# Kernel optimization log

Hardware: AMD Instinct MI355X
Metric: run time of the kernel (lower is better)

Reference implementation:

```python
import jax, jax.numpy as jnp
import numpy as np
import math

D_MODEL = 768
NUM_HEADS = 12
HEAD_DIM = D_MODEL // NUM_HEADS
HIDDEN = 3072
EPS = 1e-05
CLAMP = 1e9


def setup_inputs() -> dict:
    key = jax.random.key(0)
    ks = jax.random.split(key, 8)
    s = 0.02
    return {
        "x": jax.random.normal(ks[0], (1, 4096, D_MODEL), dtype=jnp.float32),
        "gamma1": jnp.ones((D_MODEL,), jnp.float32),
        "beta1": jnp.zeros((D_MODEL,), jnp.float32),
        "Wqkv": jax.random.normal(ks[1], (D_MODEL, 3 * D_MODEL), jnp.float32) * s,
        "bqkv": jnp.zeros((3 * D_MODEL,), jnp.float32),
        "Wo": jax.random.normal(ks[2], (D_MODEL, D_MODEL), jnp.float32) * s,
        "bo": jnp.zeros((D_MODEL,), jnp.float32),
        "gamma2": jnp.ones((D_MODEL,), jnp.float32),
        "beta2": jnp.zeros((D_MODEL,), jnp.float32),
        "W1": jax.random.normal(ks[3], (D_MODEL, HIDDEN), jnp.float32) * s,
        "b1": jnp.zeros((HIDDEN,), jnp.float32),
        "W2": jax.random.normal(ks[4], (HIDDEN, D_MODEL), jnp.float32) * s,
        "b2": jnp.zeros((D_MODEL,), jnp.float32),
    }


def layer_norm(x, gamma, beta):
    mean = jnp.mean(x, axis=-1, keepdims=True)
    var = jnp.mean((x - mean) ** 2, axis=-1, keepdims=True)
    y = (x - mean) / jnp.sqrt(var + EPS)
    return gamma * y + beta


def attention_block(x, Wqkv, bqkv, Wo, bo):
    B, S, D = x.shape
    qkv = x @ Wqkv + bqkv                             # [B,S,3D]
    qkv = qkv.reshape(B, S, NUM_HEADS, 3 * HEAD_DIM).transpose(0, 2, 1, 3)  # [B,H,S,3hd]
    q, k, v = jnp.split(qkv, 3, axis=-1)              # each [B,H,S,hd]
    scaled = jnp.einsum("bhqd,bhkd->bhqk", q, k) / math.sqrt(HEAD_DIM)
    causal = jnp.tril(jnp.ones((S, S), dtype=bool))
    scaled = jnp.where(causal, scaled, -jnp.inf)
    scaled = jnp.clip(scaled, -CLAMP, CLAMP)          # torch clamp turns -inf into -1e9
    attn = jax.nn.softmax(scaled, axis=-1)
    vals = jnp.einsum("bhqk,bhkd->bhqd", attn, v)     # [B,H,S,hd]
    vals = vals.transpose(0, 2, 1, 3).reshape(B, S, D)
    return vals @ Wo + bo


def ffn_block(x, W1, b1, W2, b2):
    h = jax.nn.gelu(x @ W1 + b1, approximate=False)
    return h @ W2 + b2


def reference(x, gamma1, beta1, Wqkv, bqkv, Wo, bo, gamma2, beta2, W1, b1, W2, b2):
    x = x + attention_block(layer_norm(x, gamma1, beta1), Wqkv, bqkv, Wo, bo)
    x = x + ffn_block(layer_norm(x, gamma2, beta2), W1, b1, W2, b2)
    return x
```

## Files before the change

### kernel.cpp

```cpp
#include <hip/hip_runtime.h>
#include <hip/hip_bf16.h>
#include <cmath>

using u16 = unsigned short;
typedef __bf16 bf16x8 __attribute__((ext_vector_type(8)));
typedef __bf16 bf16x2 __attribute__((ext_vector_type(2)));
typedef unsigned short u16x8 __attribute__((ext_vector_type(8)));
typedef unsigned short u16x4 __attribute__((ext_vector_type(4)));
typedef float f32x4 __attribute__((ext_vector_type(4)));

#define SEQ 4096
#define DM 768
#define NH 12
#define HD 64
#define HID 3072

__device__ __forceinline__ u16 f2bf(float f) {
    union { float f; unsigned u; } v; v.f = f;
    unsigned r = v.u + 0x7fffu + ((v.u >> 16) & 1u);
    return (u16)(r >> 16);
}

__device__ __forceinline__ unsigned pack_bf16(float a, float b) {
    union { bf16x2 v; unsigned u; } c;
    c.v[0] = (__bf16)a; c.v[1] = (__bf16)b;
    return c.u;
}

__device__ __forceinline__ float gelu_exact(float v) {
    float z = fabsf(v) * 0.70710678118654752f;
    float t = __builtin_amdgcn_rcpf(__builtin_fmaf(0.3275911f, z, 1.0f));
    float p = t * __builtin_fmaf(t, __builtin_fmaf(t, __builtin_fmaf(t,
                __builtin_fmaf(t, 1.061405429f, -1.453152027f),
                1.421413741f), -0.284496736f), 0.254829592f);
    float e = __builtin_amdgcn_exp2f(-z * z * 1.44269504088896341f);
    float erfv = __builtin_fmaf(-p, e, 1.0f);
    erfv = (v < 0.0f) ? -erfv : erfv;
    return 0.5f * v * (1.0f + erfv);
}

__device__ __forceinline__ int swz64(int row, int k) {
    return (row << 6) | ((((k >> 3) ^ row) & 7) << 3) | (k & 7);
}
__device__ __forceinline__ int swz128(int row, int k) {
    return (row << 7) | ((((k >> 3) ^ row) & 15) << 3) | (k & 7);
}

__device__ __forceinline__ void ln_row(const float* __restrict__ xr,
                                       const float* __restrict__ g,
                                       const float* __restrict__ b,
                                       u16* __restrict__ yr, int t) {
    float v0 = xr[t], v1 = xr[t + 256], v2 = xr[t + 512];
    float s = v0 + v1 + v2;
#pragma unroll
    for (int m = 32; m; m >>= 1) s += __shfl_xor(s, m);
    __shared__ float red[4], red2[4];
    int wid = t >> 6, lane = t & 63;
    if (lane == 0) red[wid] = s;
    __syncthreads();
    float mean = (red[0] + red[1] + red[2] + red[3]) * (1.0f / DM);
    float d0 = v0 - mean, d1 = v1 - mean, d2 = v2 - mean;
    float q = d0 * d0 + d1 * d1 + d2 * d2;
#pragma unroll
    for (int m = 32; m; m >>= 1) q += __shfl_xor(q, m);
    if (lane == 0) red2[wid] = q;
    __syncthreads();
    float var = (red2[0] + red2[1] + red2[2] + red2[3]) * (1.0f / DM);
    float rstd = rsqrtf(var + 1e-5f);
    yr[t]       = f2bf(d0 * rstd * g[t]       + b[t]);
    yr[t + 256] = f2bf(d1 * rstd * g[t + 256] + b[t + 256]);
    yr[t + 512] = f2bf(d2 * rstd * g[t + 512] + b[t + 512]);
}

__global__ __launch_bounds__(256) void prep_kernel(
    const float* __restrict__ x, const float* __restrict__ g1, const float* __restrict__ b1,
    const float* __restrict__ Wqkv, const float* __restrict__ Wo,
    const float* __restrict__ W1, const float* __restrict__ W2,
    u16* __restrict__ WqkvT, u16* __restrict__ WoT,
    u16* __restrict__ W1T, u16* __restrict__ W2T, u16* __restrict__ y) {
    int bid = blockIdx.x;
    if (bid < 6912) {
        const float* W; u16* Wt; int K, N, ntx, b;
        if (bid < 1728)      { W = Wqkv; Wt = WqkvT; K = 768;  N = 2304; ntx = 72; b = bid; }
        else if (bid < 2304) { W = Wo;   Wt = WoT;   K = 768;  N = 768;  ntx = 24; b = bid - 1728; }
        else if (bid < 4608) { W = W1;   Wt = W1T;   K = 768;  N = 3072; ntx = 96; b = bid - 2304; }
        else                 { W = W2;   Wt = W2T;   K = 3072; N = 768;  ntx = 24; b = bid - 4608; }
        int nb = (b % ntx) * 32, kb = (b / ntx) * 32;
        __shared__ float tile[32][33];
        int tx = threadIdx.x & 31, ty = threadIdx.x >> 5;
#pragma unroll
        for (int i = 0; i < 32; i += 8)
            tile[ty + i][tx] = W[(size_t)(kb + ty + i) * N + nb + tx];
        __syncthreads();
#pragma unroll
        for (int i = 0; i < 32; i += 8)
            Wt[(size_t)(nb + ty + i) * K + kb + tx] = f2bf(tile[tx][ty + i]);
    } else {
        int row = bid - 6912;
        ln_row(x + (size_t)row * DM, g1, b1, y + (size_t)row * DM, threadIdx.x);
    }
}

__global__ __launch_bounds__(256) void ln_kernel(const float* __restrict__ x,
                                                 const float* __restrict__ g,
                                                 const float* __restrict__ b,
                                                 u16* __restrict__ y) {
    int row = blockIdx.x;
    ln_row(x + (size_t)row * DM, g, b, y + (size_t)row * DM, threadIdx.x);
}

template<int TM, int TN>
__global__ __launch_bounds__(256) void gemm_bf16(
    const u16* __restrict__ A, const u16* __restrict__ Bt,
    const float* __restrict__ bias, const float* __restrict__ resid,
    float* __restrict__ outF, u16* __restrict__ outB, u16* __restrict__ vtg,
    int M, int N, int K, int gelu) {
    constexpr int AP = TM / 32;
    constexpr int BP = TN / 32;
    constexpr int MF = (TN == 128) ? 4 : 2;
    constexpr int NF = 2;
    __shared__ __align__(16) u16 As[2][TM * 64];
    __shared__ __align__(16) u16 Bs[2][TN * 64];
    int tid = threadIdx.x;
    int lane = tid & 63, wid = tid >> 6;
    int lr = lane & 15, hi = lane >> 4;
    int wrow = (TN == 128) ? 0 : (wid >> 1) * 32;
    int wcol = (TN == 128) ? wid * 32 : (wid & 1) * 32;

    int nwg = gridDim.x;
    int wg = (blockIdx.x & 7) * (nwg >> 3) + (blockIdx.x >> 3);
    int nbx = N / TN;
    int m0 = (wg / nbx) * TM, n0 = (wg % nbx) * TN;

    f32x4 acc[MF][NF] = {};
    int srow = tid >> 3;
    int sk = (tid & 7) << 3;
    const u16* Ag = A + (size_t)(m0 + srow) * K + sk;
    const u16* Bg = Bt + (size_t)(n0 + srow) * K + sk;

    u16x8 ar[AP], br[BP];
    auto LOAD = [&](int kt) {
#pragma unroll
        for (int p = 0; p < AP; ++p)
            ar[p] = *reinterpret_cast<const u16x8*>(Ag + (size_t)p * 32 * K + kt);
#pragma unroll
        for (int p = 0; p < BP; ++p)
            br[p] = *reinterpret_cast<const u16x8*>(Bg + (size_t)p * 32 * K + kt);
    };
    auto WRITE = [&](int buf) {
#pragma unroll
        for (int p = 0; p < AP; ++p)
            *reinterpret_cast<u16x8*>(&As[buf][swz64(srow + p * 32, sk)]) = ar[p];
#pragma unroll
        for (int p = 0; p < BP; ++p)
            *reinterpret_cast<u16x8*>(&Bs[buf][swz64(srow + p * 32, sk)]) = br[p];
    };

    int NT = K >> 6;
    LOAD(0);
    WRITE(0);
#pragma unroll 2
    for (int t = 0; t < NT; ++t) {
        if (t + 1 < NT) LOAD((t + 1) << 6);
        __syncthreads();
        const u16* as = &As[t & 1][0];
        const u16* bs = &Bs[t & 1][0];
#pragma unroll
        for (int ks = 0; ks < 2; ++ks) {
            bf16x8 af[MF], bfr[NF];
#pragma unroll
            for (int m = 0; m < MF; ++m)
                af[m] = *reinterpret_cast<const bf16x8*>(&as[swz64(wrow + m * 16 + lr, ks * 32 + hi * 8)]);
#pragma unroll
            for (int n = 0; n < NF; ++n)
                bfr[n] = *reinterpret_cast<const bf16x8*>(&bs[swz64(wcol + n * 16 + lr, ks * 32 + hi * 8)]);
            __builtin_amdgcn_s_setprio(1);
#pragma unroll
            for (int m = 0; m < MF; ++m)
#pragma unroll
                for (int n = 0; n < NF; ++n)
                    acc[m][n] = __builtin_amdgcn_mfma_f32_16x16x32_bf16(af[m], bfr[n], acc[m][n], 0, 0, 0);
            __builtin_amdgcn_s_setprio(0);
        }
        if (t + 1 < NT) WRITE((t + 1) & 1);
    }
#pragma unroll
    for (int m = 0; m < MF; ++m) {
#pragma unroll
        for (int n = 0; n < NF; ++n) {
            int col = n0 + wcol + n * 16 + lr;
            float bv = bias[col];
            u16 q4[4];
#pragma unroll
            for (int r = 0; r < 4; ++r) {
                int row = m0 + wrow + m * 16 + hi * 4 + r;
                float v = acc[m][n][r] + bv;
                if (gelu) v = gelu_exact(v);
                if (resid) v += resid[(size_t)row * N + col];
                q4[r] = f2bf(v);
                if (outF) outF[(size_t)row * N + col] = v;
                if (outB) outB[(size_t)row * N + col] = q4[r];
            }
            if (vtg) {
                int h = col / 192;
                int c = col - h * 192;
                if (c >= 128) {
                    int row0 = m0 + wrow + m * 16 + hi * 4;
                    u16x4 vv; vv[0] = q4[0]; vv[1] = q4[1]; vv[2] = q4[2]; vv[3] = q4[3];
                    *reinterpret_cast<u16x4*>(&vtg[(size_t)(h * 64 + c - 128) * SEQ + row0]) = vv;
                }
            }
        }
    }
}

__global__ __launch_bounds__(256, 2) void attn_kernel(const u16* __restrict__ qkv,
                                                      const u16* __restrict__ VtG,
                                                      u16* __restrict__ attn) {
    __shared__ __align__(16) u16 Ks[2][128 * 64];
    __shared__ __align__(16) u16 Vt[2][64 * 128];
    int tid = threadIdx.x;
    int lane = tid & 63, w = tid >> 6;
    int lr = lane & 15, hi = lane >> 4;
    int upper = hi >> 1;
    const float SCL = 0.125f * 1.44269504088896340736f;

    int bid = blockIdx.x;
    int h = bid % NH;
    int qb = (SEQ / 64 - 1) - bid / NH;

    int qrow = qb * 64 + w * 16 + lr;
    bf16x8 qf[2];
#pragma unroll
    for (int ks = 0; ks < 2; ++ks)
        qf[ks] = *reinterpret_cast<const bf16x8*>(&qkv[(size_t)qrow * 2304 + h * 192 + ks * 32 + hi * 8]);

    f32x4 acc[4] = {};
    float m_run = -INFINITY, l_run = 0.0f;

    int skvr = tid >> 3;
    int skc = (tid & 7) << 3;
    int svd = tid >> 4;
    int svk = (tid & 15) << 3;
    u16x8 kr[4], vr[4];

    auto LOADKV = [&](int kb) {
#pragma unroll
        for (int p = 0; p < 4; ++p)
            kr[p] = *reinterpret_cast<const u16x8*>(
                &qkv[(size_t)(kb * 128 + skvr + p * 32) * 2304 + h * 192 + 64 + skc]);
#pragma unroll
        for (int p = 0; p < 4; ++p)
            vr[p] = *reinterpret_cast<const u16x8*>(
                &VtG[(size_t)(h * 64 + svd + p * 16) * SEQ + kb * 128 + svk]);
    };
    auto WRITEKV = [&](int buf) {
#pragma unroll
        for (int p = 0; p < 4; ++p)
            *reinterpret_cast<u16x8*>(&Ks[buf][swz64(skvr + p * 32, skc)]) = kr[p];
#pragma unroll
        for (int p = 0; p < 4; ++p)
            *reinterpret_cast<u16x8*>(&Vt[buf][swz128(svd + p * 16, svk)]) = vr[p];
    };

    int nt = (qb * 64 + 64 + 127) >> 7;
    LOADKV(0);
    WRITEKV(0);
    for (int kb = 0; kb < nt; ++kb) {
        if (kb + 1 < nt) LOADKV(kb + 1);
        __syncthreads();
        const u16* ksb = &Ks[kb & 1][0];
        const u16* vtb = &Vt[kb & 1][0];

        f32x4 s[8] = {};
        __builtin_amdgcn_s_setprio(1);
#pragma unroll
        for (int ks = 0; ks < 2; ++ks) {
#pragma unroll
            for (int n = 0; n < 8; ++n) {
                bf16x8 kf = *reinterpret_cast<const bf16x8*>(&ksb[swz64(n * 16 + lr, ks * 32 + hi * 8)]);
                s[n] = __builtin_amdgcn_mfma_f32_16x16x32_bf16(kf, qf[ks], s[n], 0, 0, 0);
            }
        }
        __builtin_amdgcn_s_setprio(0);
        float sv[8][4];
#pragma unroll
        for (int n = 0; n < 8; ++n) {
            sv[n][0] = s[n][0]; sv[n][1] = s[n][1]; sv[n][2] = s[n][2]; sv[n][3] = s[n][3];
        }
        if (kb == nt - 1) {
#pragma unroll
            for (int n = 0; n < 8; ++n)
#pragma unroll
                for (int r = 0; r < 4; ++r) {
                    int kv = kb * 128 + n * 16 + hi * 4 + r;
                    if (kv > qrow) sv[n][r] = -3.0e38f;
                }
        }
        float t8[8];
#pragma unroll
        for (int n = 0; n < 8; ++n)
            t8[n] = fmaxf(fmaxf(sv[n][0], sv[n][1]), fmaxf(sv[n][2], sv[n][3]));
        float mx = fmaxf(fmaxf(fmaxf(t8[0], t8[1]), fmaxf(t8[2], t8[3])),
                         fmaxf(fmaxf(t8[4], t8[5]), fmaxf(t8[6], t8[7])));
        mx = fmaxf(mx, __shfl_xor(mx, 16));
        mx = fmaxf(mx, __shfl_xor(mx, 32));
        float mxs = mx * SCL;
        if (!__all(mxs <= m_run + 8.0f)) {
            float mnew = fmaxf(m_run, mxs);
            float alpha = __builtin_amdgcn_exp2f(m_run - mnew);
            l_run *= alpha;
#pragma unroll
            for (int n2 = 0; n2 < 4; ++n2)
#pragma unroll
                for (int r = 0; r < 4; ++r) acc[n2][r] *= alpha;
            m_run = mnew;
        }
        float rs = 0.0f;
#pragma unroll
        for (int n = 0; n < 8; ++n) {
            float p0 = __builtin_amdgcn_exp2f(__builtin_fmaf(sv[n][0], SCL, -m_run));
            float p1 = __builtin_amdgcn_exp2f(__builtin_fmaf(sv[n][1], SCL, -m_run));
            float p2 = __builtin_amdgcn_exp2f(__builtin_fmaf(sv[n][2], SCL, -m_run));
            float p3 = __builtin_amdgcn_exp2f(__builtin_fmaf(sv[n][3], SCL, -m_run));
            sv[n][0] = p0; sv[n][1] = p1; sv[n][2] = p2; sv[n][3] = p3;
            rs += (p0 + p1) + (p2 + p3);
        }
        rs += __shfl_xor(rs, 16);
        rs += __shfl_xor(rs, 32);
        l_run += rs;

        unsigned pk0[8], pk1[8];
#pragma unroll
        for (int n = 0; n < 8; ++n) {
            pk0[n] = pack_bf16(sv[n][0], sv[n][1]);
            pk1[n] = pack_bf16(sv[n][2], sv[n][3]);
        }
        int src0 = lr + ((hi & 1) << 5);
        int src1 = src0 + 16;
#pragma unroll
        for (int ks = 0; ks < 4; ++ks) {
            union { unsigned w4[4]; bf16x8 v; } pf;
            {
                unsigned a0 = __shfl(pk0[2 * ks], src0), b0 = __shfl(pk0[2 * ks + 1], src0);
                unsigned a1 = __shfl(pk1[2 * ks], src0), b1 = __shfl(pk1[2 * ks + 1], src0);
                unsigned a2 = __shfl(pk0[2 * ks], src1), b2 = __shfl(pk0[2 * ks + 1], src1);
                unsigned a3 = __shfl(pk1[2 * ks], src1), b3 = __shfl(pk1[2 * ks + 1], src1);
                pf.w4[0] = upper ? b0 : a0;
                pf.w4[1] = upper ? b1 : a1;
                pf.w4[2] = upper ? b2 : a2;
                pf.w4[3] = upper ? b3 : a3;
            }
            __builtin_amdgcn_s_setprio(1);
#pragma unroll
            for (int n2 = 0; n2 < 4; ++n2) {
                bf16x8 vf = *reinterpret_cast<const bf16x8*>(&vtb[swz128(n2 * 16 + lr, ks * 32 + hi * 8)]);
                acc[n2] = __builtin_amdgcn_mfma_f32_16x16x32_bf16(vf, pf.v, acc[n2], 0, 0, 0);
            }
            __builtin_amdgcn_s_setprio(0);
        }
        if (kb + 1 < nt) WRITEKV((kb + 1) & 1);
    }
    float inv = 1.0f / l_run;
#pragma unroll
    for (int n2 = 0; n2 < 4; ++n2) {
#pragma unroll
        for (int r = 0; r < 4; ++r) {
            int dcol = h * 64 + n2 * 16 + hi * 4 + r;
            attn[(size_t)qrow * DM + dcol] = f2bf(acc[n2][r] * inv);
        }
    }
}

extern "C" void kernel_launch(void* const* d_in, const int* in_sizes, int n_in,
                              void* d_out, int out_size, void* d_ws, size_t ws_size,
                              hipStream_t stream) {
    const float* x      = (const float*)d_in[0];
    const float* gamma1 = (const float*)d_in[1];
    const float* beta1  = (const float*)d_in[2];
    const float* Wqkv   = (const float*)d_in[3];
    const float* bqkv   = (const float*)d_in[4];
    const float* Wo     = (const float*)d_in[5];
    const float* bo     = (const float*)d_in[6];
    const float* gamma2 = (const float*)d_in[7];
    const float* beta2  = (const float*)d_in[8];
    const float* W1     = (const float*)d_in[9];
    const float* b1     = (const float*)d_in[10];
    const float* W2     = (const float*)d_in[11];
    const float* b2     = (const float*)d_in[12];

    char* ws = (char*)d_ws;
    size_t off = 0;
    u16* WqkvT = (u16*)(ws + off); off += (size_t)2304 * 768 * 2;
    u16* WoT   = (u16*)(ws + off); off += (size_t)768 * 768 * 2;
    u16* W1T   = (u16*)(ws + off); off += (size_t)3072 * 768 * 2;
    u16* W2T   = (u16*)(ws + off); off += (size_t)768 * 3072 * 2;
    u16* B1    = (u16*)(ws + off); off += (size_t)SEQ * DM * 2;
    u16* Q     = (u16*)(ws + off); off += (size_t)SEQ * HID * 2;
    float* x1  = (float*)(ws + off); off += (size_t)SEQ * DM * 4;

    u16* VtG = (u16*)x1;

    prep_kernel<<<dim3(11008), 256, 0, stream>>>(x, gamma1, beta1, Wqkv, Wo, W1, W2,
                                                 WqkvT, WoT, W1T, W2T, B1);
    gemm_bf16<64, 128><<<dim3(1152), 256, 0, stream>>>(B1, WqkvT, bqkv, nullptr, nullptr, Q, VtG, SEQ, 2304, 768, 0);
    attn_kernel<<<dim3((SEQ / 64) * NH), 256, 0, stream>>>(Q, VtG, B1);
    gemm_bf16<64, 64><<<dim3(768), 256, 0, stream>>>(B1, WoT, bo, x, x1, nullptr, nullptr, SEQ, 768, 768, 0);
    ln_kernel<<<SEQ, 256, 0, stream>>>(x1, gamma2, beta2, B1);
    gemm_bf16<64, 128><<<dim3(1536), 256, 0, stream>>>(B1, W1T, b1, nullptr, nullptr, Q, nullptr, SEQ, 3072, 768, 1);
    gemm_bf16<64, 64><<<dim3(768), 256, 0, stream>>>(Q, W2T, b2, x1, (float*)d_out, nullptr, nullptr, SEQ, 768, 3072, 0);
}
```

Before: 206.4 us.

## Stage GEMM tiles with direct global-to-LDS loads and deeper prefetch

The GEMM kernel now uses global_load_lds to copy A/B tiles straight into shared memory, with the swizzle applied on the global address side. Tiles are prefetched two k-steps ahead and synchronised with explicit vmcnt waits and barriers. This removes the register staging and the LDS write instructions. The launch also switches from a 1D grid with XCD-aware block remapping to a plain 2D grid, which may hurt L2 locality across chiplets.

```diff
diff --git a/kernel.cpp b/kernel.cpp
--- a/kernel.cpp
+++ b/kernel.cpp
@@ -14,6 +14,10 @@
 #define NH 12
 #define HD 64
 #define HID 3072
+
+#define GLD_LDS16(g, l) __builtin_amdgcn_global_load_lds( \
+    (const __attribute__((address_space(1))) void*)(g),   \
+    (__attribute__((address_space(3))) void*)(l), 16, 0, 0)
 
 __device__ __forceinline__ u16 f2bf(float f) {
     union { float f; unsigned u; } v; v.f = f;
@@ -115,8 +119,9 @@
     const float* __restrict__ bias, const float* __restrict__ resid,
     float* __restrict__ outF, u16* __restrict__ outB, u16* __restrict__ vtg,
     int M, int N, int K, int gelu) {
-    constexpr int AP = TM / 32;
-    constexpr int BP = TN / 32;
+    constexpr int APR = TM / 32;
+    constexpr int BPR = TN / 32;
+    constexpr int GL = APR + BPR;
     constexpr int MF = (TN == 128) ? 4 : 2;
     constexpr int NF = 2;
     __shared__ __align__(16) u16 As[2][TM * 64];
@@ -126,43 +131,34 @@
     int lr = lane & 15, hi = lane >> 4;
     int wrow = (TN == 128) ? 0 : (wid >> 1) * 32;
     int wcol = (TN == 128) ? wid * 32 : (wid & 1) * 32;
-
-    int nwg = gridDim.x;
-    int wg = (blockIdx.x & 7) * (nwg >> 3) + (blockIdx.x >> 3);
-    int nbx = N / TN;
-    int m0 = (wg / nbx) * TM, n0 = (wg % nbx) * TN;
+    int m0 = blockIdx.y * TM, n0 = blockIdx.x * TN;
 
     f32x4 acc[MF][NF] = {};
-    int srow = tid >> 3;
-    int sk = (tid & 7) << 3;
-    const u16* Ag = A + (size_t)(m0 + srow) * K + sk;
-    const u16* Bg = Bt + (size_t)(n0 + srow) * K + sk;
-
-    u16x8 ar[AP], br[BP];
-    auto LOAD = [&](int kt) {
-#pragma unroll
-        for (int p = 0; p < AP; ++p)
-            ar[p] = *reinterpret_cast<const u16x8*>(Ag + (size_t)p * 32 * K + kt);
-#pragma unroll
-        for (int p = 0; p < BP; ++p)
-            br[p] = *reinterpret_cast<const u16x8*>(Bg + (size_t)p * 32 * K + kt);
+    int rsub = wid * 8 + (lane >> 3);
+    int chunk = lane & 7;
+
+    auto STAGE = [&](int buf, int kt) {
+#pragma unroll
+        for (int p = 0; p < APR; ++p) {
+            int row = p * 32 + rsub;
+            int col = kt + (((chunk ^ row) & 7) << 3);
+            GLD_LDS16(A + (size_t)(m0 + row) * K + col, &As[buf][(p * 32 + wid * 8) * 64]);
+        }
+#pragma unroll
+        for (int p = 0; p < BPR; ++p) {
+            int row = p * 32 + rsub;
+            int col = kt + (((chunk ^ row) & 7) << 3);
+            GLD_LDS16(Bt + (size_t)(n0 + row) * K + col, &Bs[buf][(p * 32 + wid * 8) * 64]);
+        }
     };
-    auto WRITE = [&](int buf) {
-#pragma unroll
-        for (int p = 0; p < AP; ++p)
-            *reinterpret_cast<u16x8*>(&As[buf][swz64(srow + p * 32, sk)]) = ar[p];
-#pragma unroll
-        for (int p = 0; p < BP; ++p)
-            *reinterpret_cast<u16x8*>(&Bs[buf][swz64(srow + p * 32, sk)]) = br[p];
-    };
 
     int NT = K >> 6;
-    LOAD(0);
-    WRITE(0);
-#pragma unroll 2
+    STAGE(0, 0);
+    STAGE(1, 64);
     for (int t = 0; t < NT; ++t) {
-        if (t + 1 < NT) LOAD((t + 1) << 6);
-        __syncthreads();
+        if (t + 1 < NT) asm volatile("s_waitcnt vmcnt(%0)" :: "i"(GL) : "memory");
+        else            asm volatile("s_waitcnt vmcnt(0)" ::: "memory");
+        __builtin_amdgcn_s_barrier();
         const u16* as = &As[t & 1][0];
         const u16* bs = &Bs[t & 1][0];
 #pragma unroll
@@ -182,7 +178,8 @@
                     acc[m][n] = __builtin_amdgcn_mfma_f32_16x16x32_bf16(af[m], bfr[n], acc[m][n], 0, 0, 0);
             __builtin_amdgcn_s_setprio(0);
         }
-        if (t + 1 < NT) WRITE((t + 1) & 1);
+        __builtin_amdgcn_s_barrier();
+        if (t + 2 < NT) STAGE(t & 1, (t + 2) << 6);
     }
 #pragma unroll
     for (int m = 0; m < MF; ++m) {
@@ -403,10 +400,10 @@
 
     prep_kernel<<<dim3(11008), 256, 0, stream>>>(x, gamma1, beta1, Wqkv, Wo, W1, W2,
                                                  WqkvT, WoT, W1T, W2T, B1);
-    gemm_bf16<64, 128><<<dim3(1152), 256, 0, stream>>>(B1, WqkvT, bqkv, nullptr, nullptr, Q, VtG, SEQ, 2304, 768, 0);
+    gemm_bf16<64, 128><<<dim3(2304 / 128, SEQ / 64), 256, 0, stream>>>(B1, WqkvT, bqkv, nullptr, nullptr, Q, VtG, SEQ, 2304, 768, 0);
     attn_kernel<<<dim3((SEQ / 64) * NH), 256, 0, stream>>>(Q, VtG, B1);
-    gemm_bf16<64, 64><<<dim3(768), 256, 0, stream>>>(B1, WoT, bo, x, x1, nullptr, nullptr, SEQ, 768, 768, 0);
+    gemm_bf16<64, 64><<<dim3(768 / 64, SEQ / 64), 256, 0, stream>>>(B1, WoT, bo, x, x1, nullptr, nullptr, SEQ, 768, 768, 0);
     ln_kernel<<<SEQ, 256, 0, stream>>>(x1, gamma2, beta2, B1);
-    gemm_bf16<64, 128><<<dim3(1536), 256, 0, stream>>>(B1, W1T, b1, nullptr, nullptr, Q, nullptr, SEQ, 3072, 768, 1);
-    gemm_bf16<64, 64><<<dim3(768), 256, 0, stream>>>(Q, W2T, b2, x1, (float*)d_out, nullptr, nullptr, SEQ, 768, 3072, 0);
-}
+    gemm_bf16<64, 128><<<dim3(3072 / 128, SEQ / 64), 256, 0, stream>>>(B1, W1T, b1, nullptr, nullptr, Q, nullptr, SEQ, 3072, 768, 1);
+    gemm_bf16<64, 64><<<dim3(768 / 64, SEQ / 64), 256, 0, stream>>>(Q, W2T, b2, x1, (float*)d_out, nullptr, nullptr, SEQ, 768, 3072, 0);
+}
```

Result: no change. 206.8 us (+0.2%).
